# Kernel optimization log

Hardware: AMD Instinct MI355X
Metric: run time of the kernel (lower is better)

## Reference

```python
import jax, jax.numpy as jnp
import numpy as np

CUTOFF = 5.0
MAX_NUM_PAIRS = 131072
N_ATOMS = 4096
BOX_L = 40.0


def setup_inputs() -> dict:
    key = jax.random.key(0)
    k1, _ = jax.random.split(key)
    positions = jax.random.uniform(k1, (N_ATOMS, 3), dtype=jnp.float32) * BOX_L
    box = jnp.eye(3, dtype=jnp.float32) * BOX_L  # triclinic box vectors (rows)
    return {"positions": positions, "box": box}


def _min_image_deltas(positions, box):
    # delta[i, j] = positions[i] - positions[j], wrapped by the minimum image
    # convention: subtract the nearest integer multiple of the box vectors.
    delta = positions[:, None, :] - positions[None, :, :]  # [N, N, 3]
    inv_box = jnp.linalg.inv(box)
    frac = delta @ inv_box                                  # fractional coords
    delta = delta - jnp.round(frac) @ box
    return delta


def reference(positions, box):
    n = positions.shape[0]
    delta = _min_image_deltas(positions, box)               # [N, N, 3]
    dist2 = jnp.sum(delta * delta, axis=-1)                 # [N, N]

    idx = jnp.arange(n)
    upper = idx[:, None] < idx[None, :]                     # unique pairs i<j
    mask = upper & (dist2 < CUTOFF * CUTOFF)

    n_pairs = jnp.sum(mask).astype(jnp.int32)
    # Compact hit pairs into a fixed-size buffer (static shape for jit).
    flat_idx, = jnp.nonzero(mask.ravel(), size=MAX_NUM_PAIRS, fill_value=0)
    valid = jnp.arange(MAX_NUM_PAIRS) < n_pairs

    pair_i = jnp.where(valid, flat_idx // n, -1)
    pair_j = jnp.where(valid, flat_idx % n, -1)
    pairs = jnp.stack([pair_i, pair_j], axis=0)             # [2, P]

    deltas = jnp.where(valid[:, None], delta.reshape(n * n, 3)[flat_idx], 0.0)
    d2 = jnp.where(valid, dist2.ravel()[flat_idx], 1.0)     # safe sqrt on pads
    distances = jnp.where(valid, jnp.sqrt(d2), 0.0)

    return pairs, deltas, distances, n_pairs
```

## Files before the change

### kernel.cpp

```cpp
#include <hip/hip_runtime.h>


#define CUT2 25.0f

__device__ __forceinline__ void load_box_inv(const float* __restrict__ box,
                                             float B[3][3], float Binv[3][3]) {
    #pragma unroll
    for (int r = 0; r < 3; ++r)
        #pragma unroll
        for (int c = 0; c < 3; ++c)
            B[r][c] = box[r * 3 + c];

    float a00 = B[0][0], a01 = B[0][1], a02 = B[0][2];
    float a10 = B[1][0], a11 = B[1][1], a12 = B[1][2];
    float a20 = B[2][0], a21 = B[2][1], a22 = B[2][2];

    float adj00 =  (a11 * a22 - a12 * a21);
    float adj01 = -(a01 * a22 - a02 * a21);
    float adj02 =  (a01 * a12 - a02 * a11);
    float adj10 = -(a10 * a22 - a12 * a20);
    float adj11 =  (a00 * a22 - a02 * a20);
    float adj12 = -(a00 * a12 - a02 * a10);
    float adj20 =  (a10 * a21 - a11 * a20);
    float adj21 = -(a00 * a21 - a01 * a20);
    float adj22 =  (a00 * a11 - a01 * a10);

    float det = a00 * adj00 + a01 * adj10 + a02 * adj20;

    Binv[0][0] = __fdiv_rn(adj00, det); Binv[0][1] = __fdiv_rn(adj01, det); Binv[0][2] = __fdiv_rn(adj02, det);
    Binv[1][0] = __fdiv_rn(adj10, det); Binv[1][1] = __fdiv_rn(adj11, det); Binv[1][2] = __fdiv_rn(adj12, det);
    Binv[2][0] = __fdiv_rn(adj20, det); Binv[2][1] = __fdiv_rn(adj21, det); Binv[2][2] = __fdiv_rn(adj22, det);
}

__device__ __forceinline__ void min_image(float xi, float yi, float zi,
                                          float xj, float yj, float zj,
                                          const float B[3][3], const float Binv[3][3],
                                          float& dx, float& dy, float& dz, float& d2) {
    dx = __fsub_rn(xi, xj);
    dy = __fsub_rn(yi, yj);
    dz = __fsub_rn(zi, zj);

    float f0 = __fadd_rn(__fadd_rn(__fmul_rn(dx, Binv[0][0]), __fmul_rn(dy, Binv[1][0])), __fmul_rn(dz, Binv[2][0]));
    float f1 = __fadd_rn(__fadd_rn(__fmul_rn(dx, Binv[0][1]), __fmul_rn(dy, Binv[1][1])), __fmul_rn(dz, Binv[2][1]));
    float f2 = __fadd_rn(__fadd_rn(__fmul_rn(dx, Binv[0][2]), __fmul_rn(dy, Binv[1][2])), __fmul_rn(dz, Binv[2][2]));

    float r0 = rintf(f0), r1 = rintf(f1), r2 = rintf(f2);

    float c0 = __fadd_rn(__fadd_rn(__fmul_rn(r0, B[0][0]), __fmul_rn(r1, B[1][0])), __fmul_rn(r2, B[2][0]));
    float c1 = __fadd_rn(__fadd_rn(__fmul_rn(r0, B[0][1]), __fmul_rn(r1, B[1][1])), __fmul_rn(r2, B[2][1]));
    float c2 = __fadd_rn(__fadd_rn(__fmul_rn(r0, B[0][2]), __fmul_rn(r1, B[1][2])), __fmul_rn(r2, B[2][2]));

    dx = __fsub_rn(dx, c0);
    dy = __fsub_rn(dy, c1);
    dz = __fsub_rn(dz, c2);

    d2 = __fadd_rn(__fadd_rn(__fmul_rn(dx, dx), __fmul_rn(dy, dy)), __fmul_rn(dz, dz));
}

__device__ __forceinline__ void min_image_diag(float xi, float yi, float zi,
                                               float xj, float yj, float zj,
                                               float b0, float b1, float b2,
                                               float ib0, float ib1, float ib2,
                                               float& dx, float& dy, float& dz, float& d2) {
    dx = __fsub_rn(xi, xj);
    dy = __fsub_rn(yi, yj);
    dz = __fsub_rn(zi, zj);
    float r0 = rintf(__fmul_rn(dx, ib0));
    float r1 = rintf(__fmul_rn(dy, ib1));
    float r2 = rintf(__fmul_rn(dz, ib2));
    dx = __fsub_rn(dx, __fmul_rn(r0, b0));
    dy = __fsub_rn(dy, __fmul_rn(r1, b1));
    dz = __fsub_rn(dz, __fmul_rn(r2, b2));
    d2 = __fadd_rn(__fadd_rn(__fmul_rn(dx, dx), __fmul_rn(dy, dy)), __fmul_rn(dz, dz));
}

__global__ void __launch_bounds__(256)
k0_transpose(const float* __restrict__ pos,
             float* __restrict__ X, float* __restrict__ Y, float* __restrict__ Z,
             int N) {
    int idx = blockIdx.x * blockDim.x + threadIdx.x;
    if (idx < N) {
        X[idx] = pos[3 * idx + 0];
        Y[idx] = pos[3 * idx + 1];
        Z[idx] = pos[3 * idx + 2];
    }
}

template <bool DIAG>
__device__ __forceinline__ int count_row(int i, int lane,
                                         const float* __restrict__ X,
                                         const float* __restrict__ Y,
                                         const float* __restrict__ Z,
                                         const float B[3][3], const float Binv[3][3],
                                         unsigned long long* __restrict__ mrow,
                                         int nchunks) {
    float xi = X[i], yi = Y[i], zi = Z[i];
    float b0 = B[0][0], b1 = B[1][1], b2 = B[2][2];
    float ib0 = Binv[0][0], ib1 = Binv[1][1], ib2 = Binv[2][2];
    int c0 = i >> 6;
    int cnt = 0;

    {
        int j = (c0 << 6) + lane;
        bool hit = false;
        if (j > i) {
            float dx, dy, dz, d2;
            if (DIAG)
                min_image_diag(xi, yi, zi, X[j], Y[j], Z[j],
                               b0, b1, b2, ib0, ib1, ib2, dx, dy, dz, d2);
            else
                min_image(xi, yi, zi, X[j], Y[j], Z[j], B, Binv, dx, dy, dz, d2);
            hit = (d2 < CUT2);
        }
        unsigned long long m = __ballot(hit);
        if (lane == 0) mrow[c0] = m;
        cnt += __popcll(m);
    }

    int c = c0 + 1;
    for (; c + 4 <= nchunks; c += 4) {
        int j0 = (c << 6) + lane;
        float dx0, dy0, dz0, d20, dx1, dy1, dz1, d21;
        float dx2, dy2, dz2, d22, dx3, dy3, dz3, d23;
        if (DIAG) {
            min_image_diag(xi, yi, zi, X[j0 +   0], Y[j0 +   0], Z[j0 +   0], b0, b1, b2, ib0, ib1, ib2, dx0, dy0, dz0, d20);
            min_image_diag(xi, yi, zi, X[j0 +  64], Y[j0 +  64], Z[j0 +  64], b0, b1, b2, ib0, ib1, ib2, dx1, dy1, dz1, d21);
            min_image_diag(xi, yi, zi, X[j0 + 128], Y[j0 + 128], Z[j0 + 128], b0, b1, b2, ib0, ib1, ib2, dx2, dy2, dz2, d22);
            min_image_diag(xi, yi, zi, X[j0 + 192], Y[j0 + 192], Z[j0 + 192], b0, b1, b2, ib0, ib1, ib2, dx3, dy3, dz3, d23);
        } else {
            min_image(xi, yi, zi, X[j0 +   0], Y[j0 +   0], Z[j0 +   0], B, Binv, dx0, dy0, dz0, d20);
            min_image(xi, yi, zi, X[j0 +  64], Y[j0 +  64], Z[j0 +  64], B, Binv, dx1, dy1, dz1, d21);
            min_image(xi, yi, zi, X[j0 + 128], Y[j0 + 128], Z[j0 + 128], B, Binv, dx2, dy2, dz2, d22);
            min_image(xi, yi, zi, X[j0 + 192], Y[j0 + 192], Z[j0 + 192], B, Binv, dx3, dy3, dz3, d23);
        }
        unsigned long long m0 = __ballot(d20 < CUT2);
        unsigned long long m1 = __ballot(d21 < CUT2);
        unsigned long long m2 = __ballot(d22 < CUT2);
        unsigned long long m3 = __ballot(d23 < CUT2);
        if (lane == 0) { mrow[c] = m0; mrow[c + 1] = m1; mrow[c + 2] = m2; mrow[c + 3] = m3; }
        cnt += __popcll(m0) + __popcll(m1) + __popcll(m2) + __popcll(m3);
    }
    for (; c < nchunks; ++c) {
        int j = (c << 6) + lane;
        float dx, dy, dz, d2;
        if (DIAG)
            min_image_diag(xi, yi, zi, X[j], Y[j], Z[j],
                           b0, b1, b2, ib0, ib1, ib2, dx, dy, dz, d2);
        else
            min_image(xi, yi, zi, X[j], Y[j], Z[j], B, Binv, dx, dy, dz, d2);
        unsigned long long m = __ballot(d2 < CUT2);
        if (lane == 0) mrow[c] = m;
        cnt += __popcll(m);
    }
    return cnt;
}

__global__ void __launch_bounds__(256)
k1_pad_count(const float* __restrict__ X, const float* __restrict__ Y,
             const float* __restrict__ Z, const float* __restrict__ box,
             float* __restrict__ out, int* __restrict__ counts,
             unsigned long long* __restrict__ masks, int N, int P) {
    int tid = blockIdx.x * blockDim.x + threadIdx.x;
    int nthreads = gridDim.x * blockDim.x;

    int total = 6 * P + 1;
    for (int k = tid; k < total; k += nthreads)
        out[k] = (k < 2 * P) ? -1.0f : 0.0f;

    int i = tid >> 6;
    int lane = tid & 63;
    int nchunks = N >> 6;

    float B[3][3], Binv[3][3];
    load_box_inv(box, B, Binv);
    bool diag = (B[0][1] == 0.0f) & (B[0][2] == 0.0f) & (B[1][0] == 0.0f) &
                (B[1][2] == 0.0f) & (B[2][0] == 0.0f) & (B[2][1] == 0.0f);

    int cnt;
    if (diag)
        cnt = count_row<true>(i, lane, X, Y, Z, B, Binv,
                              masks + (size_t)i * nchunks, nchunks);
    else
        cnt = count_row<false>(i, lane, X, Y, Z, B, Binv,
                               masks + (size_t)i * nchunks, nchunks);
    if (lane == 0) counts[i] = cnt;
}

__global__ void __launch_bounds__(256)
k2_scan_fill(const float* __restrict__ X, const float* __restrict__ Y,
             const float* __restrict__ Z, const float* __restrict__ box,
             const int* __restrict__ counts,
             const unsigned long long* __restrict__ masks,
             float* __restrict__ out, int N, int P) {
    int tid = blockIdx.x * blockDim.x + threadIdx.x;
    int i = tid >> 6;
    int lane = tid & 63;
    int nchunks = N >> 6;
    int c0 = i >> 6;

    int pre = 0;
    for (int base = 0; base < i; base += 256) {
        int idx = base + 4 * lane;
        int4 v = *(const int4*)(counts + idx);
        if (idx + 0 < i) pre += v.x;
        if (idx + 1 < i) pre += v.y;
        if (idx + 2 < i) pre += v.z;
        if (idx + 3 < i) pre += v.w;
    }
    #pragma unroll
    for (int d = 1; d < 64; d <<= 1)
        pre += __shfl_xor(pre, d);

    if (i == N - 1 && lane == 0)
        out[6 * (size_t)P] = (float)(pre + counts[i]);

    unsigned long long mymask = masks[(size_t)i * nchunks + lane];

    float B[3][3], Binv[3][3];
    load_box_inv(box, B, Binv);
    float xi = X[i], yi = Y[i], zi = Z[i];

    int base = pre;
    for (int cc = c0; cc < nchunks; ++cc) {
        unsigned long long m = __shfl(mymask, cc);
        if (m != 0ull) {
            if ((m >> lane) & 1ull) {
                int j = (cc << 6) + lane;
                float dx, dy, dz, d2;
                min_image(xi, yi, zi, X[j], Y[j], Z[j], B, Binv, dx, dy, dz, d2);
                int slot = base + __popcll(m & ((1ull << lane) - 1ull));
                if (slot < P) {
                    out[slot] = (float)i;
                    out[P + slot] = (float)j;
                    size_t db = 2 * (size_t)P + 3 * (size_t)slot;
                    out[db + 0] = dx;
                    out[db + 1] = dy;
                    out[db + 2] = dz;
                    out[5 * (size_t)P + slot] = sqrtf(d2);
                }
            }
            base += __popcll(m);
        }
    }
}

extern "C" void kernel_launch(void* const* d_in, const int* in_sizes, int n_in,
                              void* d_out, int out_size, void* d_ws, size_t ws_size,
                              hipStream_t stream) {
    const float* pos = (const float*)d_in[0];
    const float* box = (const float*)d_in[1];
    float* out = (float*)d_out;

    int N = in_sizes[0] / 3;
    int P = (out_size - 1) / 6;
    int nchunks = N >> 6;

    char* w = (char*)d_ws;
    float* X = (float*)w;                          w += (size_t)N * sizeof(float);
    float* Y = (float*)w;                          w += (size_t)N * sizeof(float);
    float* Z = (float*)w;                          w += (size_t)N * sizeof(float);
    int* counts = (int*)w;                         w += (size_t)N * sizeof(int);
    unsigned long long* masks = (unsigned long long*)w;

    k0_transpose<<<(N + 255) / 256, 256, 0, stream>>>(pos, X, Y, Z, N);

    k1_pad_count<<<N / 4, 256, 0, stream>>>(X, Y, Z, box, out, counts, masks, N, P);

    k2_scan_fill<<<N / 4, 256, 0, stream>>>(X, Y, Z, box, counts, masks, out, N, P);
}
```

Before: 87.01 us.

## Use cell list to restrict pair search to neighboring cells

Adds a single-block cell-list build that bins atoms into up to 8x8x8 periodic cells and sorts their coordinates. The count kernel then scans only the 27 neighboring cells per atom instead of all N, setting mask bits with atomicOr after zeroing the bitmask in a prep kernel. This trades O(N^2) distance work for a serial single-block build, a full zeroing of the 2 MB mask buffer, and scattered global atomics. Non-diagonal or small boxes fall back to the full scan.

Result: slower. 115.7 us (+33.0%).

```diff
diff --git a/kernel.cpp b/kernel.cpp
--- a/kernel.cpp
+++ b/kernel.cpp
@@ -2,6 +2,8 @@
 
 
 #define CUT2 25.0f
+#define CUTOFF 5.0f
+#define MAXC 512
 
 __device__ __forceinline__ void load_box_inv(const float* __restrict__ box,
                                              float B[3][3], float Binv[3][3]) {
@@ -30,6 +32,37 @@
     Binv[0][0] = __fdiv_rn(adj00, det); Binv[0][1] = __fdiv_rn(adj01, det); Binv[0][2] = __fdiv_rn(adj02, det);
     Binv[1][0] = __fdiv_rn(adj10, det); Binv[1][1] = __fdiv_rn(adj11, det); Binv[1][2] = __fdiv_rn(adj12, det);
     Binv[2][0] = __fdiv_rn(adj20, det); Binv[2][1] = __fdiv_rn(adj21, det); Binv[2][2] = __fdiv_rn(adj22, det);
+}
+
+__device__ __forceinline__ bool box_is_diag(const float B[3][3]) {
+    return (B[0][1] == 0.0f) & (B[0][2] == 0.0f) & (B[1][0] == 0.0f) &
+           (B[1][2] == 0.0f) & (B[2][0] == 0.0f) & (B[2][1] == 0.0f) &
+           (B[0][0] > 0.0f) & (B[1][1] > 0.0f) & (B[2][2] > 0.0f);
+}
+
+__device__ __forceinline__ bool cell_params(const float B[3][3],
+                                            int& ncx, int& ncy, int& ncz,
+                                            float& ivx, float& ivy, float& ivz) {
+    float margin = CUTOFF * 1.001f;
+    ncx = (int)(B[0][0] / margin);
+    ncy = (int)(B[1][1] / margin);
+    ncz = (int)(B[2][2] / margin);
+    if (ncx < 3 || ncy < 3 || ncz < 3) return false;
+    if (ncx > 8) ncx = 8;
+    if (ncy > 8) ncy = 8;
+    if (ncz > 8) ncz = 8;
+    ivx = (float)ncx / B[0][0];
+    ivy = (float)ncy / B[1][1];
+    ivz = (float)ncz / B[2][2];
+    return true;
+}
+
+__device__ __forceinline__ int cell_of_dim(float u, float L, float inv, int nc) {
+    u = u - L * floorf(u / L);
+    int c = (int)(u * inv);
+    if (c < 0) c = 0;
+    if (c >= nc) c = nc - 1;
+    return c;
 }
 
 __device__ __forceinline__ void min_image(float xi, float yi, float zi,
@@ -75,31 +108,94 @@
 }
 
 __global__ void __launch_bounds__(256)
-k0_transpose(const float* __restrict__ pos,
-             float* __restrict__ X, float* __restrict__ Y, float* __restrict__ Z,
-             int N) {
-    int idx = blockIdx.x * blockDim.x + threadIdx.x;
-    if (idx < N) {
-        X[idx] = pos[3 * idx + 0];
-        Y[idx] = pos[3 * idx + 1];
-        Z[idx] = pos[3 * idx + 2];
+k0_prep(const float* __restrict__ pos,
+        float* __restrict__ X, float* __restrict__ Y, float* __restrict__ Z,
+        unsigned long long* __restrict__ masks,
+        float* __restrict__ out, int N, int P) {
+    int tid = blockIdx.x * blockDim.x + threadIdx.x;
+    int nthreads = gridDim.x * blockDim.x;
+
+    int total = 6 * P + 1;
+    for (int k = tid; k < total; k += nthreads)
+        out[k] = (k < 2 * P) ? -1.0f : 0.0f;
+
+    int nwords = N * (N >> 6) / 64;
+    nwords = N * (N >> 6);
+    for (int k = tid; k < nwords; k += nthreads)
+        masks[k] = 0ull;
+
+    if (tid < N) {
+        X[tid] = pos[3 * tid + 0];
+        Y[tid] = pos[3 * tid + 1];
+        Z[tid] = pos[3 * tid + 2];
+    }
+}
+
+__global__ void __launch_bounds__(1024)
+kbuild(const float* __restrict__ box,
+       const float* __restrict__ X, const float* __restrict__ Y,
+       const float* __restrict__ Z,
+       int* __restrict__ cellstart, int* __restrict__ jid,
+       float* __restrict__ Xs, float* __restrict__ Ys, float* __restrict__ Zs,
+       int N) {
+    __shared__ int hist[MAXC];
+    __shared__ int cur[MAXC];
+
+    float B[3][3], Binv[3][3];
+    load_box_inv(box, B, Binv);
+    int ncx, ncy, ncz; float ivx, ivy, ivz;
+    if (!box_is_diag(B) || !cell_params(B, ncx, ncy, ncz, ivx, ivy, ivz))
+        return;
+    int nc3 = ncx * ncy * ncz;
+
+    int tid = threadIdx.x;
+    for (int c = tid; c < nc3; c += 1024) hist[c] = 0;
+    __syncthreads();
+
+    for (int a = tid; a < N; a += 1024) {
+        int cx = cell_of_dim(X[a], B[0][0], ivx, ncx);
+        int cy = cell_of_dim(Y[a], B[1][1], ivy, ncy);
+        int cz = cell_of_dim(Z[a], B[2][2], ivz, ncz);
+        atomicAdd(&hist[(cz * ncy + cy) * ncx + cx], 1);
+    }
+    __syncthreads();
+
+    if (tid == 0) {
+        int run = 0;
+        for (int c = 0; c < nc3; ++c) {
+            cellstart[c] = run;
+            cur[c] = run;
+            run += hist[c];
+        }
+        cellstart[nc3] = run;
+    }
+    __syncthreads();
+
+    for (int a = tid; a < N; a += 1024) {
+        int cx = cell_of_dim(X[a], B[0][0], ivx, ncx);
+        int cy = cell_of_dim(Y[a], B[1][1], ivy, ncy);
+        int cz = cell_of_dim(Z[a], B[2][2], ivz, ncz);
+        int s = atomicAdd(&cur[(cz * ncy + cy) * ncx + cx], 1);
+        jid[s] = a;
+        Xs[s] = X[a];
+        Ys[s] = Y[a];
+        Zs[s] = Z[a];
     }
 }
 
 template <bool DIAG>
-__device__ __forceinline__ int count_row(int i, int lane,
-                                         const float* __restrict__ X,
-                                         const float* __restrict__ Y,
-                                         const float* __restrict__ Z,
-                                         const float B[3][3], const float Binv[3][3],
-                                         unsigned long long* __restrict__ mrow,
-                                         int nchunks) {
+__device__ __forceinline__ int count_row_full(int i, int lane,
+                                              const float* __restrict__ X,
+                                              const float* __restrict__ Y,
+                                              const float* __restrict__ Z,
+                                              const float B[3][3], const float Binv[3][3],
+                                              unsigned long long* __restrict__ mrow,
+                                              int nchunks) {
     float xi = X[i], yi = Y[i], zi = Z[i];
     float b0 = B[0][0], b1 = B[1][1], b2 = B[2][2];
     float ib0 = Binv[0][0], ib1 = Binv[1][1], ib2 = Binv[2][2];
     int c0 = i >> 6;
     int cnt = 0;
-
     {
         int j = (c0 << 6) + lane;
         bool hit = false;
@@ -116,31 +212,7 @@
         if (lane == 0) mrow[c0] = m;
         cnt += __popcll(m);
     }
-
-    int c = c0 + 1;
-    for (; c + 4 <= nchunks; c += 4) {
-        int j0 = (c << 6) + lane;
-        float dx0, dy0, dz0, d20, dx1, dy1, dz1, d21;
-        float dx2, dy2, dz2, d22, dx3, dy3, dz3, d23;
-        if (DIAG) {
-            min_image_diag(xi, yi, zi, X[j0 +   0], Y[j0 +   0], Z[j0 +   0], b0, b1, b2, ib0, ib1, ib2, dx0, dy0, dz0, d20);
-            min_image_diag(xi, yi, zi, X[j0 +  64], Y[j0 +  64], Z[j0 +  64], b0, b1, b2, ib0, ib1, ib2, dx1, dy1, dz1, d21);
-            min_image_diag(xi, yi, zi, X[j0 + 128], Y[j0 + 128], Z[j0 + 128], b0, b1, b2, ib0, ib1, ib2, dx2, dy2, dz2, d22);
-            min_image_diag(xi, yi, zi, X[j0 + 192], Y[j0 + 192], Z[j0 + 192], b0, b1, b2, ib0, ib1, ib2, dx3, dy3, dz3, d23);
-        } else {
-            min_image(xi, yi, zi, X[j0 +   0], Y[j0 +   0], Z[j0 +   0], B, Binv, dx0, dy0, dz0, d20);
-            min_image(xi, yi, zi, X[j0 +  64], Y[j0 +  64], Z[j0 +  64], B, Binv, dx1, dy1, dz1, d21);
-            min_image(xi, yi, zi, X[j0 + 128], Y[j0 + 128], Z[j0 + 128], B, Binv, dx2, dy2, dz2, d22);
-            min_image(xi, yi, zi, X[j0 + 192], Y[j0 + 192], Z[j0 + 192], B, Binv, dx3, dy3, dz3, d23);
-        }
-        unsigned long long m0 = __ballot(d20 < CUT2);
-        unsigned long long m1 = __ballot(d21 < CUT2);
-        unsigned long long m2 = __ballot(d22 < CUT2);
-        unsigned long long m3 = __ballot(d23 < CUT2);
-        if (lane == 0) { mrow[c] = m0; mrow[c + 1] = m1; mrow[c + 2] = m2; mrow[c + 3] = m3; }
-        cnt += __popcll(m0) + __popcll(m1) + __popcll(m2) + __popcll(m3);
-    }
-    for (; c < nchunks; ++c) {
+    for (int c = c0 + 1; c < nchunks; ++c) {
         int j = (c << 6) + lane;
         float dx, dy, dz, d2;
         if (DIAG)
@@ -156,34 +228,75 @@
 }
 
 __global__ void __launch_bounds__(256)
-k1_pad_count(const float* __restrict__ X, const float* __restrict__ Y,
-             const float* __restrict__ Z, const float* __restrict__ box,
-             float* __restrict__ out, int* __restrict__ counts,
-             unsigned long long* __restrict__ masks, int N, int P) {
+k1_count(const float* __restrict__ X, const float* __restrict__ Y,
+         const float* __restrict__ Z, const float* __restrict__ box,
+         const int* __restrict__ cellstart, const int* __restrict__ jid,
+         const float* __restrict__ Xs, const float* __restrict__ Ys,
+         const float* __restrict__ Zs,
+         int* __restrict__ counts, unsigned long long* __restrict__ masks,
+         int N, int P) {
     int tid = blockIdx.x * blockDim.x + threadIdx.x;
-    int nthreads = gridDim.x * blockDim.x;
-
-    int total = 6 * P + 1;
-    for (int k = tid; k < total; k += nthreads)
-        out[k] = (k < 2 * P) ? -1.0f : 0.0f;
-
     int i = tid >> 6;
     int lane = tid & 63;
     int nchunks = N >> 6;
 
     float B[3][3], Binv[3][3];
     load_box_inv(box, B, Binv);
-    bool diag = (B[0][1] == 0.0f) & (B[0][2] == 0.0f) & (B[1][0] == 0.0f) &
-                (B[1][2] == 0.0f) & (B[2][0] == 0.0f) & (B[2][1] == 0.0f);
-
-    int cnt;
-    if (diag)
-        cnt = count_row<true>(i, lane, X, Y, Z, B, Binv,
-                              masks + (size_t)i * nchunks, nchunks);
-    else
-        cnt = count_row<false>(i, lane, X, Y, Z, B, Binv,
-                               masks + (size_t)i * nchunks, nchunks);
-    if (lane == 0) counts[i] = cnt;
+    bool diag = box_is_diag(B);
+    int ncx, ncy, ncz; float ivx, ivy, ivz;
+    bool cells = diag && cell_params(B, ncx, ncy, ncz, ivx, ivy, ivz);
+
+    unsigned long long* mrow = masks + (size_t)i * nchunks;
+
+    if (cells) {
+        float xi = X[i], yi = Y[i], zi = Z[i];
+        float b0 = B[0][0], b1 = B[1][1], b2 = B[2][2];
+        float ib0 = Binv[0][0], ib1 = Binv[1][1], ib2 = Binv[2][2];
+        int icx = cell_of_dim(xi, b0, ivx, ncx);
+        int icy = cell_of_dim(yi, b1, ivy, ncy);
+        int icz = cell_of_dim(zi, b2, ivz, ncz);
+
+        int cnt = 0;
+        #pragma unroll
+        for (int dz = -1; dz <= 1; ++dz) {
+            int cz = icz + dz; cz += (cz < 0) ? ncz : 0; cz -= (cz >= ncz) ? ncz : 0;
+            #pragma unroll
+            for (int dy = -1; dy <= 1; ++dy) {
+                int cy = icy + dy; cy += (cy < 0) ? ncy : 0; cy -= (cy >= ncy) ? ncy : 0;
+                #pragma unroll
+                for (int dx = -1; dx <= 1; ++dx) {
+                    int cx = icx + dx; cx += (cx < 0) ? ncx : 0; cx -= (cx >= ncx) ? ncx : 0;
+                    int c = (cz * ncy + cy) * ncx + cx;
+                    int s = cellstart[c], e = cellstart[c + 1];
+                    for (int off = s; off < e; off += 64) {
+                        int k = off + lane;
+                        bool hit = false;
+                        int j = 0;
+                        if (k < e) {
+                            j = jid[k];
+                            float ddx, ddy, ddz, d2;
+                            min_image_diag(xi, yi, zi, Xs[k], Ys[k], Zs[k],
+                                           b0, b1, b2, ib0, ib1, ib2,
+                                           ddx, ddy, ddz, d2);
+                            hit = (d2 < CUT2) & (j > i);
+                        }
+                        unsigned long long m = __ballot(hit);
+                        cnt += __popcll(m);
+                        if (hit)
+                            atomicOr(&mrow[j >> 6], 1ull << (j & 63));
+                    }
+                }
+            }
+        }
+        if (lane == 0) counts[i] = cnt;
+    } else {
+        int cnt;
+        if (diag)
+            cnt = count_row_full<true>(i, lane, X, Y, Z, B, Binv, mrow, nchunks);
+        else
+            cnt = count_row_full<false>(i, lane, X, Y, Z, B, Binv, mrow, nchunks);
+        if (lane == 0) counts[i] = cnt;
+    }
 }
 
 __global__ void __launch_bounds__(256)
@@ -261,10 +374,16 @@
     float* Z = (float*)w;                          w += (size_t)N * sizeof(float);
     int* counts = (int*)w;                         w += (size_t)N * sizeof(int);
     unsigned long long* masks = (unsigned long long*)w;
-
-    k0_transpose<<<(N + 255) / 256, 256, 0, stream>>>(pos, X, Y, Z, N);
-
-    k1_pad_count<<<N / 4, 256, 0, stream>>>(X, Y, Z, box, out, counts, masks, N, P);
-
+                                                   w += (size_t)N * nchunks * sizeof(unsigned long long);
+    int* cellstart = (int*)w;                      w += (size_t)(MAXC + 1) * sizeof(int);
+    int* jid = (int*)w;                            w += (size_t)N * sizeof(int);
+    float* Xs = (float*)w;                         w += (size_t)N * sizeof(float);
+    float* Ys = (float*)w;                         w += (size_t)N * sizeof(float);
+    float* Zs = (float*)w;
+
+    k0_prep<<<1024, 256, 0, stream>>>(pos, X, Y, Z, masks, out, N, P);
+    kbuild<<<1, 1024, 0, stream>>>(box, X, Y, Z, cellstart, jid, Xs, Ys, Zs, N);
+    k1_count<<<N / 4, 256, 0, stream>>>(X, Y, Z, box, cellstart, jid, Xs, Ys, Zs,
+                                        counts, masks, N, P);
     k2_scan_fill<<<N / 4, 256, 0, stream>>>(X, Y, Z, box, counts, masks, out, N, P);
 }
```
